# Kernel tuning notes

Hardware: AMD Instinct MI355X
Metric: run time of the kernel (lower is better)

Reference implementation:

```python
import jax, jax.numpy as jnp
import numpy as np

N, M, D, L = 8, 2048, 128, 128  # batch, num_nodes, input_dim, latent_dim


def setup_inputs() -> dict:
    key = jax.random.key(0)
    ks = jax.random.split(key, 9)
    s = 0.02
    return {
        "x": jax.random.normal(ks[0], (N, M, D), dtype=jnp.float32),
        # f_node: Linear(D, 2L) -> ReLU -> Linear(2L, L)
        "w1n": jax.random.normal(ks[1], (D, 2 * L), dtype=jnp.float32) * s,
        "b1n": jnp.zeros((2 * L,), dtype=jnp.float32),
        "w2n": jax.random.normal(ks[2], (2 * L, L), dtype=jnp.float32) * s,
        "b2n": jnp.zeros((L,), dtype=jnp.float32),
        # f_edge: Linear(2L, L) -> ReLU -> Linear(L, 1)
        "w1e": jax.random.normal(ks[3], (2 * L, L), dtype=jnp.float32) * s,
        "b1e": jnp.zeros((L,), dtype=jnp.float32),
        "w2e": jax.random.normal(ks[4], (L, 1), dtype=jnp.float32) * s,
        "b2e": jnp.zeros((1,), dtype=jnp.float32),
    }


def reference(x, w1n, b1n, w2n, b2n, w1e, b1e, w2e, b2e):
    n, m, _ = x.shape
    # f_node MLP: (N, m, D) -> (N, m, L)
    h = jnp.maximum(x @ w1n + b1n, 0.0) @ w2n + b2n
    # In the original, the double transpose on `receiver` cancels, so the
    # edge feature is concat(x_i, x_i) for every (i, j) pair: independent of j.
    # Compute per-node then broadcast across j (identical math, no O(m^2 * 2L) blowup).
    pair = jnp.concatenate([h, h], axis=-1)              # (N, m, 2L)
    e = jnp.maximum(pair @ w1e + b1e, 0.0) @ w2e + b2e   # (N, m, 1)
    e = e / m
    edge = jnp.broadcast_to(e, (n, m, m))                # edge[b, i, j] = e[b, i]
    return h, edge
```

## Files before the change

### kernel.cpp

```cpp
#include <hip/hip_runtime.h>


typedef short short8 __attribute__((ext_vector_type(8)));
typedef float floatx4 __attribute__((ext_vector_type(4)));

__device__ __forceinline__ short f2bf(float f) {
    union { float f; unsigned u; } v; v.f = f;
    unsigned r = v.u + 0x7fffu + ((v.u >> 16) & 1u);
    return (short)(r >> 16);
}

__global__ __launch_bounds__(256)
void prep_weights(const float* __restrict__ w1n, const float* __restrict__ w2n,
                  const float* __restrict__ w1e, short* __restrict__ ws)
{
    const int id = blockIdx.x * 256 + threadIdx.x;
    const int j = id & 7;
    if (id < 32768) {
        const int g = id >> 3, l = g & 63, ctk = g >> 6;
        const int ct = ctk >> 2, k = ctk & 3;
        const int kg = k * 32 + (l >> 4) * 8 + j;
        ws[id] = f2bf(w1n[kg * 256 + ct * 16 + (l & 15)]);
    } else if (id < 65536) {
        const int g = (id - 32768) >> 3, l = g & 63, ctk = g >> 6;
        const int ct = ctk >> 3, k = ctk & 7;
        const int kg = k * 32 + (l >> 4) * 8 + j;
        ws[id] = f2bf(w2n[kg * 128 + ct * 16 + (l & 15)]);
    } else {
        const int g = (id - 65536) >> 3, l = g & 63, ctk = g >> 6;
        const int ct = ctk >> 2, k = ctk & 3;
        const int kg = k * 32 + (l >> 4) * 8 + j;
        ws[id] = f2bf(w1e[kg * 128 + ct * 16 + (l & 15)]
                      + w1e[(kg + 128) * 128 + ct * 16 + (l & 15)]);
    }
}

#define TPB 256
#define H1_STRIDE 264
#define HB_STRIDE 136

__global__ __launch_bounds__(TPB, 4)
void node_compute(const float* __restrict__ x,
                  const float* __restrict__ b1n, const float* __restrict__ b2n,
                  const float* __restrict__ b1e,
                  const float* __restrict__ w2e, const float* __restrict__ b2e,
                  const short* __restrict__ wt,
                  float* __restrict__ h_out, float* __restrict__ e_ws)
{
    __shared__ short h1s[16 * H1_STRIDE];
    __shared__ short hbs[16 * HB_STRIDE];
    __shared__ float partial[4][16];

    const int t = threadIdx.x;
    const int w = t >> 6;
    const int l = t & 63;
    const int l15 = l & 15;
    const int quad = l >> 4;
    const int row0 = blockIdx.x * 16;

    const short* __restrict__ W2S = wt + 32768;
    const short* __restrict__ WES = wt + 65536;

    short8 a1[4];
#pragma unroll
    for (int k = 0; k < 4; ++k) {
        const float* p = x + (size_t)(row0 + l15) * 128 + k * 32 + quad * 8;
        const float4 v0 = *(const float4*)p;
        const float4 v1 = *(const float4*)(p + 4);
        short8 a;
        a[0] = f2bf(v0.x); a[1] = f2bf(v0.y); a[2] = f2bf(v0.z); a[3] = f2bf(v0.w);
        a[4] = f2bf(v1.x); a[5] = f2bf(v1.y); a[6] = f2bf(v1.z); a[7] = f2bf(v1.w);
        a1[k] = a;
    }

#pragma unroll
    for (int ci = 0; ci < 4; ++ci) {
        const int ct = 4 * w + ci;
        const float b = b1n[ct * 16 + l15];
        floatx4 acc = (floatx4){b, b, b, b};
#pragma unroll
        for (int k = 0; k < 4; ++k) {
            const short8 bf = *(const short8*)(wt + ((ct * 4 + k) * 64 + l) * 8);
            acc = __builtin_amdgcn_mfma_f32_16x16x32_bf16(a1[k], bf, acc, 0, 0, 0);
        }
#pragma unroll
        for (int r = 0; r < 4; ++r)
            h1s[(quad * 4 + r) * H1_STRIDE + ct * 16 + l15] = f2bf(fmaxf(acc[r], 0.f));
    }
    __syncthreads();

    short8 a2[8];
#pragma unroll
    for (int k = 0; k < 8; ++k)
        a2[k] = *(const short8*)&h1s[l15 * H1_STRIDE + k * 32 + quad * 8];

#pragma unroll
    for (int ci = 0; ci < 2; ++ci) {
        const int ct = 2 * w + ci;
        const float b = b2n[ct * 16 + l15];
        floatx4 acc = (floatx4){b, b, b, b};
#pragma unroll
        for (int k = 0; k < 8; ++k) {
            const short8 bf = *(const short8*)(W2S + ((ct * 8 + k) * 64 + l) * 8);
            acc = __builtin_amdgcn_mfma_f32_16x16x32_bf16(a2[k], bf, acc, 0, 0, 0);
        }
#pragma unroll
        for (int r = 0; r < 4; ++r) {
            const int row = quad * 4 + r;
            h_out[(size_t)(row0 + row) * 128 + ct * 16 + l15] = acc[r];
            hbs[row * HB_STRIDE + ct * 16 + l15] = f2bf(acc[r]);
        }
    }
    __syncthreads();

    short8 a3[4];
#pragma unroll
    for (int k = 0; k < 4; ++k)
        a3[k] = *(const short8*)&hbs[l15 * HB_STRIDE + k * 32 + quad * 8];

    float p[4] = {0.f, 0.f, 0.f, 0.f};
#pragma unroll
    for (int ci = 0; ci < 2; ++ci) {
        const int ct = 2 * w + ci;
        const float b = b1e[ct * 16 + l15];
        floatx4 acc = (floatx4){b, b, b, b};
#pragma unroll
        for (int k = 0; k < 4; ++k) {
            const short8 bf = *(const short8*)(WES + ((ct * 4 + k) * 64 + l) * 8);
            acc = __builtin_amdgcn_mfma_f32_16x16x32_bf16(a3[k], bf, acc, 0, 0, 0);
        }
        const float wv = w2e[ct * 16 + l15];
#pragma unroll
        for (int r = 0; r < 4; ++r)
            p[r] += fmaxf(acc[r], 0.f) * wv;
    }
#pragma unroll
    for (int off = 8; off >= 1; off >>= 1)
#pragma unroll
        for (int r = 0; r < 4; ++r)
            p[r] += __shfl_xor(p[r], off, 64);
    if (l15 == 0) {
#pragma unroll
        for (int r = 0; r < 4; ++r)
            partial[w][quad * 4 + r] = p[r];
    }
    __syncthreads();
    if (t < 16) {
        e_ws[row0 + t] = (partial[0][t] + partial[1][t] + partial[2][t]
                          + partial[3][t] + b2e[0]) * (1.0f / 2048.0f);
    }
}

__global__ __launch_bounds__(256)
void edge_broadcast(const float* __restrict__ es, float* __restrict__ edge_out)
{
    const int t = threadIdx.x;
    const int r0 = blockIdx.x * 2;
    const float v0 = es[r0];
    const float v1 = es[r0 + 1];
    floatx4* __restrict__ e4 = (floatx4*)(edge_out + (size_t)r0 * 2048);
    const floatx4 a = (floatx4){v0, v0, v0, v0};
    const floatx4 b = (floatx4){v1, v1, v1, v1};
    e4[t] = a;
    e4[t + 256] = a;
    e4[t + 512] = b;
    e4[t + 768] = b;
}

extern "C" void kernel_launch(void* const* d_in, const int* in_sizes, int n_in,
                              void* d_out, int out_size, void* d_ws, size_t ws_size,
                              hipStream_t stream) {
    const float* x   = (const float*)d_in[0];
    const float* w1n = (const float*)d_in[1];
    const float* b1n = (const float*)d_in[2];
    const float* w2n = (const float*)d_in[3];
    const float* b2n = (const float*)d_in[4];
    const float* w1e = (const float*)d_in[5];
    const float* b1e = (const float*)d_in[6];
    const float* w2e = (const float*)d_in[7];
    const float* b2e = (const float*)d_in[8];

    float* h_out    = (float*)d_out;
    float* edge_out = (float*)d_out + (size_t)8 * 2048 * 128;
    short* wt       = (short*)d_ws;
    float* e_ws     = (float*)((char*)d_ws + 163840);

    prep_weights<<<dim3(320), dim3(256), 0, stream>>>(w1n, w2n, w1e, wt);
    node_compute<<<dim3(1024), dim3(TPB), 0, stream>>>(
        x, b1n, b2n, b1e, w2e, b2e, wt, h_out, e_ws);
    edge_broadcast<<<dim3(2048), dim3(256), 0, stream>>>(e_ws, edge_out);
}
```

Measured before the change: 158.0 us.

## Fuse edge broadcast into node kernel and process 32 rows per block

```diff
diff --git a/kernel.cpp b/kernel.cpp
--- a/kernel.cpp
+++ b/kernel.cpp
@@ -36,135 +36,157 @@
 }
 
 #define TPB 256
+#define RPB 32
 #define H1_STRIDE 264
 #define HB_STRIDE 136
 
-__global__ __launch_bounds__(TPB, 4)
-void node_compute(const float* __restrict__ x,
-                  const float* __restrict__ b1n, const float* __restrict__ b2n,
-                  const float* __restrict__ b1e,
-                  const float* __restrict__ w2e, const float* __restrict__ b2e,
-                  const short* __restrict__ wt,
-                  float* __restrict__ h_out, float* __restrict__ e_ws)
+__global__ __launch_bounds__(TPB, 2)
+void node_edge(const float* __restrict__ x,
+               const float* __restrict__ b1n, const float* __restrict__ b2n,
+               const float* __restrict__ b1e,
+               const float* __restrict__ w2e, const float* __restrict__ b2e,
+               const short* __restrict__ wt,
+               float* __restrict__ h_out, float* __restrict__ edge_out)
 {
-    __shared__ short h1s[16 * H1_STRIDE];
-    __shared__ short hbs[16 * HB_STRIDE];
-    __shared__ float partial[4][16];
+    __shared__ short h1s[RPB * H1_STRIDE];
+    __shared__ short hbs[RPB * HB_STRIDE];
+    __shared__ float partial[4][RPB];
+    __shared__ float es_s[RPB];
 
     const int t = threadIdx.x;
     const int w = t >> 6;
     const int l = t & 63;
     const int l15 = l & 15;
     const int quad = l >> 4;
-    const int row0 = blockIdx.x * 16;
+    const int row0 = blockIdx.x * RPB;
 
     const short* __restrict__ W2S = wt + 32768;
     const short* __restrict__ WES = wt + 65536;
 
-    short8 a1[4];
-#pragma unroll
-    for (int k = 0; k < 4; ++k) {
-        const float* p = x + (size_t)(row0 + l15) * 128 + k * 32 + quad * 8;
-        const float4 v0 = *(const float4*)p;
-        const float4 v1 = *(const float4*)(p + 4);
-        short8 a;
-        a[0] = f2bf(v0.x); a[1] = f2bf(v0.y); a[2] = f2bf(v0.z); a[3] = f2bf(v0.w);
-        a[4] = f2bf(v1.x); a[5] = f2bf(v1.y); a[6] = f2bf(v1.z); a[7] = f2bf(v1.w);
-        a1[k] = a;
-    }
-
-#pragma unroll
-    for (int ci = 0; ci < 4; ++ci) {
-        const int ct = 4 * w + ci;
-        const float b = b1n[ct * 16 + l15];
-        floatx4 acc = (floatx4){b, b, b, b};
+    short8 wf1[16];
+#pragma unroll
+    for (int ci = 0; ci < 4; ++ci)
+#pragma unroll
+        for (int k = 0; k < 4; ++k)
+            wf1[ci * 4 + k] =
+                *(const short8*)(wt + (((4 * w + ci) * 4 + k) * 64 + l) * 8);
+
+#pragma unroll
+    for (int rt = 0; rt < 2; ++rt) {
+        short8 a1[4];
 #pragma unroll
         for (int k = 0; k < 4; ++k) {
-            const short8 bf = *(const short8*)(wt + ((ct * 4 + k) * 64 + l) * 8);
-            acc = __builtin_amdgcn_mfma_f32_16x16x32_bf16(a1[k], bf, acc, 0, 0, 0);
-        }
-#pragma unroll
-        for (int r = 0; r < 4; ++r)
-            h1s[(quad * 4 + r) * H1_STRIDE + ct * 16 + l15] = f2bf(fmaxf(acc[r], 0.f));
-    }
-    __syncthreads();
-
-    short8 a2[8];
-#pragma unroll
-    for (int k = 0; k < 8; ++k)
-        a2[k] = *(const short8*)&h1s[l15 * H1_STRIDE + k * 32 + quad * 8];
-
-#pragma unroll
-    for (int ci = 0; ci < 2; ++ci) {
-        const int ct = 2 * w + ci;
-        const float b = b2n[ct * 16 + l15];
-        floatx4 acc = (floatx4){b, b, b, b};
-#pragma unroll
-        for (int k = 0; k < 8; ++k) {
-            const short8 bf = *(const short8*)(W2S + ((ct * 8 + k) * 64 + l) * 8);
-            acc = __builtin_amdgcn_mfma_f32_16x16x32_bf16(a2[k], bf, acc, 0, 0, 0);
-        }
-#pragma unroll
-        for (int r = 0; r < 4; ++r) {
-            const int row = quad * 4 + r;
-            h_out[(size_t)(row0 + row) * 128 + ct * 16 + l15] = acc[r];
-            hbs[row * HB_STRIDE + ct * 16 + l15] = f2bf(acc[r]);
-        }
-    }
-    __syncthreads();
-
-    short8 a3[4];
-#pragma unroll
-    for (int k = 0; k < 4; ++k)
-        a3[k] = *(const short8*)&hbs[l15 * HB_STRIDE + k * 32 + quad * 8];
-
-    float p[4] = {0.f, 0.f, 0.f, 0.f};
-#pragma unroll
-    for (int ci = 0; ci < 2; ++ci) {
-        const int ct = 2 * w + ci;
-        const float b = b1e[ct * 16 + l15];
-        floatx4 acc = (floatx4){b, b, b, b};
-#pragma unroll
-        for (int k = 0; k < 4; ++k) {
-            const short8 bf = *(const short8*)(WES + ((ct * 4 + k) * 64 + l) * 8);
-            acc = __builtin_amdgcn_mfma_f32_16x16x32_bf16(a3[k], bf, acc, 0, 0, 0);
-        }
-        const float wv = w2e[ct * 16 + l15];
-#pragma unroll
-        for (int r = 0; r < 4; ++r)
-            p[r] += fmaxf(acc[r], 0.f) * wv;
-    }
-#pragma unroll
-    for (int off = 8; off >= 1; off >>= 1)
-#pragma unroll
-        for (int r = 0; r < 4; ++r)
-            p[r] += __shfl_xor(p[r], off, 64);
-    if (l15 == 0) {
-#pragma unroll
-        for (int r = 0; r < 4; ++r)
-            partial[w][quad * 4 + r] = p[r];
-    }
-    __syncthreads();
-    if (t < 16) {
-        e_ws[row0 + t] = (partial[0][t] + partial[1][t] + partial[2][t]
-                          + partial[3][t] + b2e[0]) * (1.0f / 2048.0f);
-    }
-}
-
-__global__ __launch_bounds__(256)
-void edge_broadcast(const float* __restrict__ es, float* __restrict__ edge_out)
-{
-    const int t = threadIdx.x;
-    const int r0 = blockIdx.x * 2;
-    const float v0 = es[r0];
-    const float v1 = es[r0 + 1];
-    floatx4* __restrict__ e4 = (floatx4*)(edge_out + (size_t)r0 * 2048);
-    const floatx4 a = (floatx4){v0, v0, v0, v0};
-    const floatx4 b = (floatx4){v1, v1, v1, v1};
-    e4[t] = a;
-    e4[t + 256] = a;
-    e4[t + 512] = b;
-    e4[t + 768] = b;
+            const float* p = x + (size_t)(row0 + rt * 16 + l15) * 128 + k * 32 + quad * 8;
+            const float4 v0 = *(const float4*)p;
+            const float4 v1 = *(const float4*)(p + 4);
+            short8 a;
+            a[0] = f2bf(v0.x); a[1] = f2bf(v0.y); a[2] = f2bf(v0.z); a[3] = f2bf(v0.w);
+            a[4] = f2bf(v1.x); a[5] = f2bf(v1.y); a[6] = f2bf(v1.z); a[7] = f2bf(v1.w);
+            a1[k] = a;
+        }
+#pragma unroll
+        for (int ci = 0; ci < 4; ++ci) {
+            const int ct = 4 * w + ci;
+            const float b = b1n[ct * 16 + l15];
+            floatx4 acc = (floatx4){b, b, b, b};
+#pragma unroll
+            for (int k = 0; k < 4; ++k)
+                acc = __builtin_amdgcn_mfma_f32_16x16x32_bf16(a1[k], wf1[ci * 4 + k], acc, 0, 0, 0);
+#pragma unroll
+            for (int r = 0; r < 4; ++r)
+                h1s[(rt * 16 + quad * 4 + r) * H1_STRIDE + ct * 16 + l15] =
+                    f2bf(fmaxf(acc[r], 0.f));
+        }
+    }
+    __syncthreads();
+
+    short8 wf2[16];
+#pragma unroll
+    for (int ci = 0; ci < 2; ++ci)
+#pragma unroll
+        for (int k = 0; k < 8; ++k)
+            wf2[ci * 8 + k] =
+                *(const short8*)(W2S + (((2 * w + ci) * 8 + k) * 64 + l) * 8);
+
+#pragma unroll
+    for (int rt = 0; rt < 2; ++rt) {
+        short8 a2[8];
+#pragma unroll
+        for (int k = 0; k < 8; ++k)
+            a2[k] = *(const short8*)&h1s[(rt * 16 + l15) * H1_STRIDE + k * 32 + quad * 8];
+#pragma unroll
+        for (int ci = 0; ci < 2; ++ci) {
+            const int ct = 2 * w + ci;
+            const float b = b2n[ct * 16 + l15];
+            floatx4 acc = (floatx4){b, b, b, b};
+#pragma unroll
+            for (int k = 0; k < 8; ++k)
+                acc = __builtin_amdgcn_mfma_f32_16x16x32_bf16(a2[k], wf2[ci * 8 + k], acc, 0, 0, 0);
+#pragma unroll
+            for (int r = 0; r < 4; ++r) {
+                const int row = rt * 16 + quad * 4 + r;
+                h_out[(size_t)(row0 + row) * 128 + ct * 16 + l15] = acc[r];
+                hbs[row * HB_STRIDE + ct * 16 + l15] = f2bf(acc[r]);
+            }
+        }
+    }
+    __syncthreads();
+
+    short8 wfe[8];
+#pragma unroll
+    for (int ci = 0; ci < 2; ++ci)
+#pragma unroll
+        for (int k = 0; k < 4; ++k)
+            wfe[ci * 4 + k] =
+                *(const short8*)(WES + (((2 * w + ci) * 4 + k) * 64 + l) * 8);
+
+#pragma unroll
+    for (int rt = 0; rt < 2; ++rt) {
+        short8 a3[4];
+#pragma unroll
+        for (int k = 0; k < 4; ++k)
+            a3[k] = *(const short8*)&hbs[(rt * 16 + l15) * HB_STRIDE + k * 32 + quad * 8];
+
+        float p[4] = {0.f, 0.f, 0.f, 0.f};
+#pragma unroll
+        for (int ci = 0; ci < 2; ++ci) {
+            const int ct = 2 * w + ci;
+            const float b = b1e[ct * 16 + l15];
+            floatx4 acc = (floatx4){b, b, b, b};
+#pragma unroll
+            for (int k = 0; k < 4; ++k)
+                acc = __builtin_amdgcn_mfma_f32_16x16x32_bf16(a3[k], wfe[ci * 4 + k], acc, 0, 0, 0);
+            const float wv = w2e[ct * 16 + l15];
+#pragma unroll
+            for (int r = 0; r < 4; ++r)
+                p[r] += fmaxf(acc[r], 0.f) * wv;
+        }
+#pragma unroll
+        for (int off = 8; off >= 1; off >>= 1)
+#pragma unroll
+            for (int r = 0; r < 4; ++r)
+                p[r] += __shfl_xor(p[r], off, 64);
+        if (l15 == 0) {
+#pragma unroll
+            for (int r = 0; r < 4; ++r)
+                partial[w][rt * 16 + quad * 4 + r] = p[r];
+        }
+    }
+    __syncthreads();
+    if (t < RPB) {
+        es_s[t] = (partial[0][t] + partial[1][t] + partial[2][t]
+                   + partial[3][t] + b2e[0]) * (1.0f / 2048.0f);
+    }
+    __syncthreads();
+
+    floatx4* __restrict__ e4 = (floatx4*)(edge_out + (size_t)row0 * 2048);
+#pragma unroll 4
+    for (int r = 0; r < RPB; ++r) {
+        const float v = es_s[r];
+        const floatx4 a = (floatx4){v, v, v, v};
+        e4[r * 512 + t] = a;
+        e4[r * 512 + t + 256] = a;
+    }
 }
 
 extern "C" void kernel_launch(void* const* d_in, const int* in_sizes, int n_in,
@@ -183,10 +205,8 @@
     float* h_out    = (float*)d_out;
     float* edge_out = (float*)d_out + (size_t)8 * 2048 * 128;
     short* wt       = (short*)d_ws;
-    float* e_ws     = (float*)((char*)d_ws + 163840);
 
     prep_weights<<<dim3(320), dim3(256), 0, stream>>>(w1n, w2n, w1e, wt);
-    node_compute<<<dim3(1024), dim3(TPB), 0, stream>>>(
-        x, b1n, b2n, b1e, w2e, b2e, wt, h_out, e_ws);
-    edge_broadcast<<<dim3(2048), dim3(256), 0, stream>>>(e_ws, edge_out);
-}
+    node_edge<<<dim3(512), dim3(TPB), 0, stream>>>(
+        x, b1n, b2n, b1e, w2e, b2e, wt, h_out, edge_out);
+}
```

Measured after the change: 170.5 us. 7.9% more time.
